# Kernel tuning notes

Measured on AMD Instinct MI355X. Metric: run time of the kernel, lower is better.

Reference implementation:

```python
import jax, jax.numpy as jnp
import numpy as np

N = 1_000_000
MU_PRIOR = 0.6447


def setup_inputs() -> dict:
    key = jax.random.key(0)
    ks = jax.random.split(key, 8)
    pred_ = jax.random.normal(ks[0], (N, 9), jnp.float32)
    Y_obs = jax.random.normal(ks[1], (N, 9), jnp.float32)
    rrs = jax.random.normal(ks[2], (N, 5), jnp.float32)
    rrs_pred = jax.random.normal(ks[3], (N, 5), jnp.float32)
    nan_array = jax.random.normal(ks[4], (N, 9), jnp.float32)  # all finite -> lens = 9
    # cov_z must be SPD so log(det(cov_z)) is finite
    A = jax.random.normal(ks[5], (N, 3, 3), jnp.float32) * 0.3
    cov_z = jnp.einsum('nij,nkj->nik', A, A) + 0.5 * jnp.eye(3, dtype=jnp.float32)
    mu_z = jax.random.normal(ks[6], (N, 3), jnp.float32)
    parameters = 1.0 + 0.01 * jax.random.normal(ks[7], (64,), jnp.float32)
    return {"pred_": pred_, "Y_obs": Y_obs, "rrs": rrs, "rrs_pred": rrs_pred,
            "nan_array": nan_array, "cov_z": cov_z, "mu_z": mu_z,
            "parameters": parameters}


def reference(pred_, Y_obs, rrs, rrs_pred, nan_array, cov_z, mu_z, parameters):
    n = pred_.shape[0]
    # --- buffers built in __init__ (default multipliers = ones) ---
    se_diag = jnp.asarray([0.0015, 0.0012, 0.001, 0.00086, 0.00057], jnp.float32) ** 2
    rrs_cov_inv = jnp.linalg.inv(jnp.diag(se_diag))            # [5,5]
    Y_cov_inv = jnp.eye(9, dtype=jnp.float32)                  # [9,9]
    s_a = jnp.eye(3, dtype=jnp.float32) * 4.9                  # [3,3]
    s_a_inv = jnp.linalg.inv(s_a)                              # [3,3]

    # trace((X) @ Cinv @ X.T) == sum_n x_n^T Cinv x_n  (trace trick, O(N))
    dr = rrs - rrs_pred                                        # [N,5]
    rrs_error = jnp.einsum('ni,ij,nj->', dr, rrs_cov_inv, dr) / (5.0 * n)

    lens = jnp.sum(~jnp.isnan(nan_array), axis=1).astype(jnp.float32)  # [N]
    dy = pred_ - Y_obs                                         # [N,9]
    obs_quad = jnp.einsum('ni,ij,nj->n', dy, Y_cov_inv, dy)    # [N]
    obs_error = jnp.sum(obs_quad / lens) / n

    # KL(N(mu_z, cov_z) || N(0.6447, s_a)) style term
    logdet_sa = jnp.log(jnp.linalg.det(s_a))
    logdet_cz = jnp.log(jnp.linalg.det(cov_z))                 # [N]
    tr_term = jnp.einsum('ij,nji->n', s_a_inv, cov_z)          # trace(s_a_inv @ cov_z)
    dm = mu_z - MU_PRIOR                                       # [N,3]
    DK = 0.5 * jnp.sum(logdet_sa - logdet_cz + tr_term) / n \
         + 0.5 * jnp.einsum('ni,ij,nj->', dm, s_a_inv, dm) / (3.0 * n)

    l2_norm = jnp.mean((parameters - 1.0) ** 2)
    return rrs_error + 10.0 * obs_error + DK + l2_norm
```

## Files before the change

kernel.cpp:

```cpp
#include <hip/hip_runtime.h>
#include <math.h>

#define MU_PRIOR   0.6447f
#define LOGDET_SA  4.767705615349743f
#define INV_SA     (1.0f/4.9f)

#define CHUNK  256
#define NF4_9  576
#define NF4_5  320
#define NF4_3  192

#define W0 (1.0f / (0.0015f  * 0.0015f))
#define W1 (1.0f / (0.0012f  * 0.0012f))
#define W2 (1.0f / (0.0010f  * 0.0010f))
#define W3 (1.0f / (0.00086f * 0.00086f))
#define W4 (1.0f / (0.00057f * 0.00057f))

__device__ __forceinline__ float warp_reduce_f(float v) {
#pragma unroll
    for (int off = 32; off > 0; off >>= 1) v += __shfl_down(v, off, 64);
    return v;
}

__device__ __forceinline__ double warp_reduce_d(double v) {
#pragma unroll
    for (int off = 32; off > 0; off >>= 1) v += __shfl_down(v, off, 64);
    return v;
}

__global__ __launch_bounds__(256) void loss_main(
    const float* __restrict__ pred, const float* __restrict__ yobs,
    const float* __restrict__ rrs,  const float* __restrict__ rrsp,
    const float* __restrict__ nanarr, const float* __restrict__ cov,
    const float* __restrict__ mu, double* __restrict__ partial)
{
    __shared__ float4 sP[NF4_9], sY[NF4_9], sN[NF4_9], sC[NF4_9];

    const int tid = threadIdx.x;
    const size_t rowBase = (size_t)blockIdx.x * CHUNK;

    const float4* gP = reinterpret_cast<const float4*>(pred   + rowBase * 9);
    const float4* gY = reinterpret_cast<const float4*>(yobs   + rowBase * 9);
    const float4* gN = reinterpret_cast<const float4*>(nanarr + rowBase * 9);
    const float4* gC = reinterpret_cast<const float4*>(cov    + rowBase * 9);
    const float4* gR = reinterpret_cast<const float4*>(rrs    + rowBase * 5);
    const float4* gQ = reinterpret_cast<const float4*>(rrsp   + rowBase * 5);
    const float4* gM = reinterpret_cast<const float4*>(mu     + rowBase * 3);

    {
        const float4 p0 = gP[tid], p1 = gP[tid + 256];
        const float4 y0 = gY[tid], y1 = gY[tid + 256];
        const float4 n0 = gN[tid], n1 = gN[tid + 256];
        const float4 c0 = gC[tid], c1 = gC[tid + 256];
        sP[tid] = p0; sP[tid + 256] = p1;
        sY[tid] = y0; sY[tid + 256] = y1;
        sN[tid] = n0; sN[tid + 256] = n1;
        sC[tid] = c0; sC[tid + 256] = c1;
        if (tid < NF4_9 - 512) {
            sP[tid + 512] = gP[tid + 512];
            sY[tid + 512] = gY[tid + 512];
            sN[tid + 512] = gN[tid + 512];
            sC[tid + 512] = gC[tid + 512];
        }
    }

    float acc = 0.0f;

    {
        const int w0 = (5 - (tid % 5)) % 5;
        float ew[5];
#pragma unroll
        for (int k = 0; k < 5; ++k) {
            int idx = w0 + k; if (idx >= 5) idx -= 5;
            ew[k] = (idx == 0) ? W0 : (idx == 1) ? W1 : (idx == 2) ? W2
                   : (idx == 3) ? W3 : W4;
        }
        float racc = 0.f;
#pragma unroll
        for (int j = 0; j < 2; ++j) {
            const int i = tid + 256 * j;
            if (j == 0 || i < NF4_5) {
                const float4 r = gR[i];
                const float4 q = gQ[i];
                const int k0 = (5 - j) % 5;
                const float d0 = r.x - q.x, d1 = r.y - q.y;
                const float d2 = r.z - q.z, d3 = r.w - q.w;
                racc += d0 * d0 * ew[(k0    ) % 5];
                racc += d1 * d1 * ew[(k0 + 1) % 5];
                racc += d2 * d2 * ew[(k0 + 2) % 5];
                racc += d3 * d3 * ew[(k0 + 3) % 5];
            }
        }
        acc += racc * 0.2f;
    }

    if (tid < NF4_3) {
        const float4 v = gM[tid];
        const float d0 = v.x - MU_PRIOR, d1 = v.y - MU_PRIOR;
        const float d2 = v.z - MU_PRIOR, d3 = v.w - MU_PRIOR;
        acc += (d0 * d0 + d1 * d1 + d2 * d2 + d3 * d3) * (1.0f / 29.4f);
    }

    __syncthreads();

    {
        const float* p = reinterpret_cast<const float*>(sP) + 9 * tid;
        const float* y = reinterpret_cast<const float*>(sY) + 9 * tid;
        const float* a = reinterpret_cast<const float*>(sN) + 9 * tid;
        const float* m = reinterpret_cast<const float*>(sC) + 9 * tid;

        float dy2 = 0.f, len = 0.f;
#pragma unroll
        for (int k = 0; k < 9; ++k) {
            const float d = p[k] - y[k];
            dy2 += d * d;
            const float v = a[k];
            len += (v == v) ? 1.0f : 0.0f;
        }
        acc += 10.0f * dy2 / len;

        const float tr  = m[0] + m[4] + m[8];
        const float det = m[0] * (m[4] * m[8] - m[5] * m[7])
                        - m[1] * (m[3] * m[8] - m[5] * m[6])
                        + m[2] * (m[3] * m[7] - m[4] * m[6]);
        acc += 0.5f * (LOGDET_SA - __logf(det) + tr * INV_SA);
    }

    acc = warp_reduce_f(acc);
    __shared__ float smem[4];
    const int lane = tid & 63;
    const int wid  = tid >> 6;
    if (lane == 0) smem[wid] = acc;
    __syncthreads();
    if (tid == 0)
        partial[blockIdx.x] = (double)(smem[0] + smem[1] + smem[2] + smem[3]);
}

__global__ __launch_bounds__(256) void loss_final(
    const double* __restrict__ partial, int nblocks,
    const float* __restrict__ params, int nparams,
    const float* __restrict__ pred, const float* __restrict__ yobs,
    const float* __restrict__ rrs,  const float* __restrict__ rrsp,
    const float* __restrict__ nanarr, const float* __restrict__ cov,
    const float* __restrict__ mu, int rows, float* __restrict__ out)
{
    const int mainRows = nblocks * CHUNK;
    double accA = 0.0;
    double accB = 0.0;

    for (int i = threadIdx.x; i < nblocks; i += 256) accA += partial[i];
    for (int i = threadIdx.x; i < nparams; i += 256) {
        const float d = params[i] - 1.0f;
        accB += (double)(d * d);
    }

    for (int r = mainRows + (int)threadIdx.x; r < rows; r += 256) {
        float dy2 = 0.f, len = 0.f;
        for (int i = 0; i < 9; ++i) {
            const float d = pred[9 * (size_t)r + i] - yobs[9 * (size_t)r + i];
            dy2 += d * d;
            const float v = nanarr[9 * (size_t)r + i];
            len += (v == v) ? 1.f : 0.f;
        }
        const float W[5] = {W0, W1, W2, W3, W4};
        float racc = 0.f;
        for (int i = 0; i < 5; ++i) {
            const float d = rrs[5 * (size_t)r + i] - rrsp[5 * (size_t)r + i];
            racc += d * d * W[i];
        }
        const float* m = cov + 9 * (size_t)r;
        const float tr  = m[0] + m[4] + m[8];
        const float det = m[0] * (m[4] * m[8] - m[5] * m[7])
                        - m[1] * (m[3] * m[8] - m[5] * m[6])
                        + m[2] * (m[3] * m[7] - m[4] * m[6]);
        float dm = 0.f;
        for (int i = 0; i < 3; ++i) {
            const float d = mu[3 * (size_t)r + i] - MU_PRIOR;
            dm += d * d;
        }
        accA += (double)(racc * 0.2f + 10.f * dy2 / len
                         + 0.5f * (LOGDET_SA - __logf(det) + tr * INV_SA)
                         + dm * (1.f / 29.4f));
    }

    double val = accA * (1.0 / (double)rows) + accB * (1.0 / (double)nparams);
    val = warp_reduce_d(val);
    __shared__ double sm[4];
    const int lane = threadIdx.x & 63;
    const int wid  = threadIdx.x >> 6;
    if (lane == 0) sm[wid] = val;
    __syncthreads();
    if (threadIdx.x == 0)
        out[0] = (float)(sm[0] + sm[1] + sm[2] + sm[3]);
}

extern "C" void kernel_launch(void* const* d_in, const int* in_sizes, int n_in,
                              void* d_out, int out_size, void* d_ws, size_t ws_size,
                              hipStream_t stream) {
    const float* pred   = (const float*)d_in[0];
    const float* yobs   = (const float*)d_in[1];
    const float* rrs    = (const float*)d_in[2];
    const float* rrsp   = (const float*)d_in[3];
    const float* nanarr = (const float*)d_in[4];
    const float* cov    = (const float*)d_in[5];
    const float* mu     = (const float*)d_in[6];
    const float* params = (const float*)d_in[7];
    float* out = (float*)d_out;

    const int rows    = in_sizes[0] / 9;
    const int nblocks = rows / CHUNK;

    double* partial = (double*)d_ws;

    if (nblocks > 0)
        loss_main<<<nblocks, 256, 0, stream>>>(pred, yobs, rrs, rrsp, nanarr,
                                               cov, mu, partial);
    loss_final<<<1, 256, 0, stream>>>(partial, nblocks, params, in_sizes[7],
                                      pred, yobs, rrs, rrsp, nanarr, cov, mu,
                                      rows, out);
}
```

Baseline: 209.5 us.

## Switch to persistent per-wave chunk loop with packed squared-diff/NaN staging

Replaces one block per 256-row chunk with a fixed grid of 2048 blocks in which each wave processes 64-row chunks in a grid-stride loop. Staging uses only wave barriers instead of block-wide syncthreads. Pred, obs and nan values are folded into one LDS array by storing the squared difference with the NaN flag in the sign bit, which cuts LDS traffic from four arrays to two. The final kernel now reduces 2048 partials. Per-wave serialized loads may expose more latency, since there are fewer outstanding requests per loop iteration.

```diff
diff --git a/kernel.cpp b/kernel.cpp
--- a/kernel.cpp
+++ b/kernel.cpp
@@ -5,10 +5,11 @@
 #define LOGDET_SA  4.767705615349743f
 #define INV_SA     (1.0f/4.9f)
 
-#define CHUNK  256
-#define NF4_9  576
-#define NF4_5  320
-#define NF4_3  192
+#define CW      64
+#define NF4C    144
+#define NF4R    80
+#define NF4M    48
+#define GRID    2048
 
 #define W0 (1.0f / (0.0015f  * 0.0015f))
 #define W1 (1.0f / (0.0012f  * 0.0012f))
@@ -28,108 +29,124 @@
     return v;
 }
 
+__device__ __forceinline__ float comb1(float p, float y, float n) {
+    const float d = p - y;
+    const float d2 = d * d;
+    const unsigned u = __float_as_uint(d2) | ((n == n) ? 0u : 0x80000000u);
+    return __uint_as_float(u);
+}
+__device__ __forceinline__ float4 comb4(float4 p, float4 y, float4 n) {
+    float4 o;
+    o.x = comb1(p.x, y.x, n.x); o.y = comb1(p.y, y.y, n.y);
+    o.z = comb1(p.z, y.z, n.z); o.w = comb1(p.w, y.w, n.w);
+    return o;
+}
+
 __global__ __launch_bounds__(256) void loss_main(
     const float* __restrict__ pred, const float* __restrict__ yobs,
     const float* __restrict__ rrs,  const float* __restrict__ rrsp,
     const float* __restrict__ nanarr, const float* __restrict__ cov,
-    const float* __restrict__ mu, double* __restrict__ partial)
+    const float* __restrict__ mu, double* __restrict__ partial, int nchunks)
 {
-    __shared__ float4 sP[NF4_9], sY[NF4_9], sN[NF4_9], sC[NF4_9];
-
-    const int tid = threadIdx.x;
-    const size_t rowBase = (size_t)blockIdx.x * CHUNK;
-
-    const float4* gP = reinterpret_cast<const float4*>(pred   + rowBase * 9);
-    const float4* gY = reinterpret_cast<const float4*>(yobs   + rowBase * 9);
-    const float4* gN = reinterpret_cast<const float4*>(nanarr + rowBase * 9);
-    const float4* gC = reinterpret_cast<const float4*>(cov    + rowBase * 9);
-    const float4* gR = reinterpret_cast<const float4*>(rrs    + rowBase * 5);
-    const float4* gQ = reinterpret_cast<const float4*>(rrsp   + rowBase * 5);
-    const float4* gM = reinterpret_cast<const float4*>(mu     + rowBase * 3);
-
-    {
-        const float4 p0 = gP[tid], p1 = gP[tid + 256];
-        const float4 y0 = gY[tid], y1 = gY[tid + 256];
-        const float4 n0 = gN[tid], n1 = gN[tid + 256];
-        const float4 c0 = gC[tid], c1 = gC[tid + 256];
-        sP[tid] = p0; sP[tid + 256] = p1;
-        sY[tid] = y0; sY[tid + 256] = y1;
-        sN[tid] = n0; sN[tid + 256] = n1;
-        sC[tid] = c0; sC[tid + 256] = c1;
-        if (tid < NF4_9 - 512) {
-            sP[tid + 512] = gP[tid + 512];
-            sY[tid + 512] = gY[tid + 512];
-            sN[tid + 512] = gN[tid + 512];
-            sC[tid + 512] = gC[tid + 512];
-        }
+    __shared__ float4 sV[4 * NF4C];
+    __shared__ float4 sC[4 * NF4C];
+
+    const int tid  = threadIdx.x;
+    const int lane = tid & 63;
+    const int wid  = tid >> 6;
+    const int wslot = wid * NF4C;
+    const int wgid  = blockIdx.x * 4 + wid;
+    const int nw    = (int)gridDim.x * 4;
+
+    const int w0 = (5 - (lane % 5)) % 5;
+    float ew[5];
+#pragma unroll
+    for (int k = 0; k < 5; ++k) {
+        int idx = w0 + k; if (idx >= 5) idx -= 5;
+        ew[k] = (idx == 0) ? W0 : (idx == 1) ? W1 : (idx == 2) ? W2
+               : (idx == 3) ? W3 : W4;
     }
 
     float acc = 0.0f;
 
-    {
-        const int w0 = (5 - (tid % 5)) % 5;
-        float ew[5];
-#pragma unroll
-        for (int k = 0; k < 5; ++k) {
-            int idx = w0 + k; if (idx >= 5) idx -= 5;
-            ew[k] = (idx == 0) ? W0 : (idx == 1) ? W1 : (idx == 2) ? W2
-                   : (idx == 3) ? W3 : W4;
-        }
-        float racc = 0.f;
-#pragma unroll
-        for (int j = 0; j < 2; ++j) {
-            const int i = tid + 256 * j;
-            if (j == 0 || i < NF4_5) {
-                const float4 r = gR[i];
-                const float4 q = gQ[i];
-                const int k0 = (5 - j) % 5;
-                const float d0 = r.x - q.x, d1 = r.y - q.y;
-                const float d2 = r.z - q.z, d3 = r.w - q.w;
-                racc += d0 * d0 * ew[(k0    ) % 5];
-                racc += d1 * d1 * ew[(k0 + 1) % 5];
-                racc += d2 * d2 * ew[(k0 + 2) % 5];
-                racc += d3 * d3 * ew[(k0 + 3) % 5];
+    for (int c = wgid; c < nchunks; c += nw) {
+        const float4* gP = reinterpret_cast<const float4*>(pred)   + (size_t)c * NF4C;
+        const float4* gY = reinterpret_cast<const float4*>(yobs)   + (size_t)c * NF4C;
+        const float4* gN = reinterpret_cast<const float4*>(nanarr) + (size_t)c * NF4C;
+        const float4* gC = reinterpret_cast<const float4*>(cov)    + (size_t)c * NF4C;
+        const float4* gR = reinterpret_cast<const float4*>(rrs)    + (size_t)c * NF4R;
+        const float4* gQ = reinterpret_cast<const float4*>(rrsp)   + (size_t)c * NF4R;
+        const float4* gM = reinterpret_cast<const float4*>(mu)     + (size_t)c * NF4M;
+
+        const float4 p0 = gP[lane], p1 = gP[lane + 64];
+        const float4 y0 = gY[lane], y1 = gY[lane + 64];
+        const float4 n0 = gN[lane], n1 = gN[lane + 64];
+        const float4 c0 = gC[lane], c1 = gC[lane + 64];
+        const float4 r0 = gR[lane], q0 = gQ[lane];
+        float4 p2, y2, n2, c2, r1, q1, m0;
+        if (lane < 16) {
+            p2 = gP[lane + 128]; y2 = gY[lane + 128];
+            n2 = gN[lane + 128]; c2 = gC[lane + 128];
+            r1 = gR[lane + 64];  q1 = gQ[lane + 64];
+        }
+        if (lane < 48) m0 = gM[lane];
+
+        {
+            float ra = 0.f;
+            const float d0 = r0.x - q0.x, d1 = r0.y - q0.y;
+            const float d2 = r0.z - q0.z, d3 = r0.w - q0.w;
+            ra += d0 * d0 * ew[0] + d1 * d1 * ew[1]
+                + d2 * d2 * ew[2] + d3 * d3 * ew[3];
+            if (lane < 16) {
+                const float e0 = r1.x - q1.x, e1 = r1.y - q1.y;
+                const float e2 = r1.z - q1.z, e3 = r1.w - q1.w;
+                ra += e0 * e0 * ew[1] + e1 * e1 * ew[2]
+                    + e2 * e2 * ew[3] + e3 * e3 * ew[4];
             }
-        }
-        acc += racc * 0.2f;
-    }
-
-    if (tid < NF4_3) {
-        const float4 v = gM[tid];
-        const float d0 = v.x - MU_PRIOR, d1 = v.y - MU_PRIOR;
-        const float d2 = v.z - MU_PRIOR, d3 = v.w - MU_PRIOR;
-        acc += (d0 * d0 + d1 * d1 + d2 * d2 + d3 * d3) * (1.0f / 29.4f);
-    }
-
-    __syncthreads();
-
-    {
-        const float* p = reinterpret_cast<const float*>(sP) + 9 * tid;
-        const float* y = reinterpret_cast<const float*>(sY) + 9 * tid;
-        const float* a = reinterpret_cast<const float*>(sN) + 9 * tid;
-        const float* m = reinterpret_cast<const float*>(sC) + 9 * tid;
-
-        float dy2 = 0.f, len = 0.f;
-#pragma unroll
-        for (int k = 0; k < 9; ++k) {
-            const float d = p[k] - y[k];
-            dy2 += d * d;
-            const float v = a[k];
-            len += (v == v) ? 1.0f : 0.0f;
-        }
-        acc += 10.0f * dy2 / len;
-
-        const float tr  = m[0] + m[4] + m[8];
-        const float det = m[0] * (m[4] * m[8] - m[5] * m[7])
-                        - m[1] * (m[3] * m[8] - m[5] * m[6])
-                        + m[2] * (m[3] * m[7] - m[4] * m[6]);
-        acc += 0.5f * (LOGDET_SA - __logf(det) + tr * INV_SA);
+            acc += ra * 0.2f;
+        }
+
+        if (lane < 48) {
+            const float d0 = m0.x - MU_PRIOR, d1 = m0.y - MU_PRIOR;
+            const float d2 = m0.z - MU_PRIOR, d3 = m0.w - MU_PRIOR;
+            acc += (d0 * d0 + d1 * d1 + d2 * d2 + d3 * d3) * (1.0f / 29.4f);
+        }
+
+        sV[wslot + lane]       = comb4(p0, y0, n0);
+        sV[wslot + lane + 64]  = comb4(p1, y1, n1);
+        sC[wslot + lane]       = c0;
+        sC[wslot + lane + 64]  = c1;
+        if (lane < 16) {
+            sV[wslot + lane + 128] = comb4(p2, y2, n2);
+            sC[wslot + lane + 128] = c2;
+        }
+
+        __builtin_amdgcn_wave_barrier();
+
+        {
+            const float* v = reinterpret_cast<const float*>(sV + wslot) + 9 * lane;
+            const float* m = reinterpret_cast<const float*>(sC + wslot) + 9 * lane;
+            float dy2 = 0.f, len = 0.f;
+#pragma unroll
+            for (int k = 0; k < 9; ++k) {
+                const unsigned u = __float_as_uint(v[k]);
+                dy2 += __uint_as_float(u & 0x7fffffffu);
+                len += (float)(1u - (u >> 31));
+            }
+            acc += 10.0f * dy2 / len;
+
+            const float tr  = m[0] + m[4] + m[8];
+            const float det = m[0] * (m[4] * m[8] - m[5] * m[7])
+                            - m[1] * (m[3] * m[8] - m[5] * m[6])
+                            + m[2] * (m[3] * m[7] - m[4] * m[6]);
+            acc += 0.5f * (LOGDET_SA - __logf(det) + tr * INV_SA);
+        }
+
+        __builtin_amdgcn_wave_barrier();
     }
 
     acc = warp_reduce_f(acc);
     __shared__ float smem[4];
-    const int lane = tid & 63;
-    const int wid  = tid >> 6;
     if (lane == 0) smem[wid] = acc;
     __syncthreads();
     if (tid == 0)
@@ -137,18 +154,18 @@
 }
 
 __global__ __launch_bounds__(256) void loss_final(
-    const double* __restrict__ partial, int nblocks,
+    const double* __restrict__ partial, int npartials,
     const float* __restrict__ params, int nparams,
     const float* __restrict__ pred, const float* __restrict__ yobs,
     const float* __restrict__ rrs,  const float* __restrict__ rrsp,
     const float* __restrict__ nanarr, const float* __restrict__ cov,
-    const float* __restrict__ mu, int rows, float* __restrict__ out)
+    const float* __restrict__ mu, int mainRows, int rows,
+    float* __restrict__ out)
 {
-    const int mainRows = nblocks * CHUNK;
     double accA = 0.0;
     double accB = 0.0;
 
-    for (int i = threadIdx.x; i < nblocks; i += 256) accA += partial[i];
+    for (int i = threadIdx.x; i < npartials; i += 256) accA += partial[i];
     for (int i = threadIdx.x; i < nparams; i += 256) {
         const float d = params[i] - 1.0f;
         accB += (double)(d * d);
@@ -207,15 +224,17 @@
     const float* params = (const float*)d_in[7];
     float* out = (float*)d_out;
 
-    const int rows    = in_sizes[0] / 9;
-    const int nblocks = rows / CHUNK;
+    const int rows     = in_sizes[0] / 9;
+    const int nchunks  = rows / CW;
+    const int mainRows = nchunks * CW;
+    int grid = (nchunks * 4 < GRID * 4) ? ((nchunks + 3) / 4 > 0 ? (nchunks + 3) / 4 : 1) : GRID;
+    if (grid > GRID) grid = GRID;
 
     double* partial = (double*)d_ws;
 
-    if (nblocks > 0)
-        loss_main<<<nblocks, 256, 0, stream>>>(pred, yobs, rrs, rrsp, nanarr,
-                                               cov, mu, partial);
-    loss_final<<<1, 256, 0, stream>>>(partial, nblocks, params, in_sizes[7],
+    loss_main<<<grid, 256, 0, stream>>>(pred, yobs, rrs, rrsp, nanarr,
+                                        cov, mu, partial, nchunks);
+    loss_final<<<1, 256, 0, stream>>>(partial, grid, params, in_sizes[7],
                                       pred, yobs, rrs, rrsp, nanarr, cov, mu,
-                                      rows, out);
-}
+                                      mainRows, rows, out);
+}
```

After: 208.2 us. About the same (-0.6%).
